# Optimization experiments

Hardware: AMD Instinct MI355X
Metric: run time of the kernel (lower is better)

The kernel has to match this reference:

```python
import jax, jax.numpy as jnp
import numpy as np

LOG2 = float(np.log(2.0))

def ssp(v):
    # shifted softplus: log(0.5*e^v + 0.5)
    return jax.nn.softplus(v) - jnp.asarray(LOG2, v.dtype)

def lora_dense(h, W, b, A, B):
    # base GEMM + per-sample (modulated) low-rank correction; scale = alpha/rank = 1
    base = jnp.einsum('b...i,io->b...o', h, W) + b
    lora = jnp.einsum('b...r,bro->b...o', jnp.einsum('b...i,bir->b...r', h, A), B)
    return ssp(base + lora)

def setup_inputs() -> dict:
    key = jax.random.key(0)
    ks = jax.random.split(key, 32)
    Bsz, Atoms, F, Rbf, R = 2, 512, 128, 64, 4
    d = {}
    d['x'] = jax.random.normal(ks[0], (Bsz, Atoms, F), jnp.float32)
    d['f_ij'] = jax.random.uniform(ks[1], (Bsz, Atoms, Atoms, Rbf), jnp.float32)
    d['c_ij'] = jax.random.uniform(ks[2], (Bsz, Atoms, Atoms), jnp.float32)
    d['mask'] = jax.random.randint(ks[3], (Bsz, Atoms, Atoms), 0, 2, jnp.int32)
    def mk(i, din, dout):
        return (jax.random.normal(ks[4+4*i], (din, dout), jnp.float32) * (1.0/np.sqrt(din)),
                jnp.zeros((dout,), jnp.float32),
                jax.random.normal(ks[5+4*i], (Bsz, din, R), jnp.float32) * 0.05,
                jax.random.normal(ks[6+4*i], (Bsz, R, dout), jnp.float32) * 0.05)
    d['W_bc'], d['b_bc'], d['A_bc'], d['B_bc'] = mk(0, F, F)      # atomwise_bc: F -> dim_filter(=F)
    d['W_f0'], d['b_f0'], d['A_f0'], d['B_f0'] = mk(1, Rbf, F)    # dis_filter layer0
    d['W_f1'], d['b_f1'], d['A_f1'], d['B_f1'] = mk(2, F, F)      # dis_filter layer1
    d['W_f2'], d['b_f2'], d['A_f2'], d['B_f2'] = mk(3, F, F)      # dis_filter layer2
    d['W_a0'], d['b_a0'], d['A_a0'], d['B_a0'] = mk(4, F, F)      # atomwise_ac layer0
    d['W_a1'], d['b_a1'], d['A_a1'], d['B_a1'] = mk(5, F, F)      # atomwise_ac layer1
    return d

def reference(x, f_ij, c_ij, mask,
              W_bc, b_bc, A_bc, B_bc,
              W_f0, b_f0, A_f0, B_f0,
              W_f1, b_f1, A_f1, B_f1,
              W_f2, b_f2, A_f2, B_f2,
              W_a0, b_a0, A_a0, B_a0,
              W_a1, b_a1, A_a1, B_a1):
    x_i = lora_dense(x, W_bc, b_bc, A_bc, B_bc)                 # (B, A, Fdim)
    h = lora_dense(f_ij, W_f0, b_f0, A_f0, B_f0)                # (B, A, A, Fdim)
    h = lora_dense(h, W_f1, b_f1, A_f1, B_f1)
    h = lora_dense(h, W_f2, b_f2, A_f2, B_f2)
    w_ij = h * c_ij[..., None]                                  # (B, A, A, Fdim)
    # x_ij = expand_dims(x_i, -3): neighbor-j features broadcast over receiver i
    y = x_i[:, None, :, :] * w_ij                               # (B, A, A, Fdim)
    y = y * mask[..., None].astype(y.dtype)
    y = jnp.sum(y, axis=-2)                                     # masked neighbor sum -> (B, A, Fdim)
    y = lora_dense(y, W_a0, b_a0, A_a0, B_a0)
    y = lora_dense(y, W_a1, b_a1, A_a1, B_a1)
    return x + y
```

## Files before the change

kernel.cpp:

```cpp
#include <hip/hip_runtime.h>
#include <hip/hip_bf16.h>


typedef float        f32x4  __attribute__((ext_vector_type(4)));
typedef unsigned int u32x4  __attribute__((ext_vector_type(4)));
typedef unsigned int u32x2  __attribute__((ext_vector_type(2)));
typedef __bf16       bf16x8 __attribute__((ext_vector_type(8)));

__device__ __forceinline__ float ssp_pre(float acc, float bpre) {
  float t = __builtin_amdgcn_exp2f(__builtin_fmaf(acc, 1.44269504089f, bpre));
  return 0.69314718056f * __builtin_amdgcn_logf(__builtin_fmaf(t, 0.5f, 0.5f));
}

__device__ __forceinline__ float ssp_f(float v) {
  float t = __builtin_amdgcn_exp2f(v * 1.44269504089f);
  return 0.69314718056f * __builtin_amdgcn_logf(__builtin_fmaf(t, 0.5f, 0.5f));
}

__device__ __forceinline__ unsigned short f2bfu(float f) {
  __hip_bfloat16 h = __float2bfloat16(f);
  return __builtin_bit_cast(unsigned short, h);
}

__device__ __forceinline__ u32x4 pack8(f32x4 a, f32x4 b) {
  u32x4 u;
  u.x = (unsigned)f2bfu(a.x) | ((unsigned)f2bfu(a.y) << 16);
  u.y = (unsigned)f2bfu(a.z) | ((unsigned)f2bfu(a.w) << 16);
  u.z = (unsigned)f2bfu(b.x) | ((unsigned)f2bfu(b.y) << 16);
  u.w = (unsigned)f2bfu(b.z) | ((unsigned)f2bfu(b.w) << 16);
  return u;
}

__device__ __forceinline__ f32x4 fzero4() { f32x4 z = {0.f, 0.f, 0.f, 0.f}; return z; }

#define SWZ(j) (((j) & 7) << 4)

__global__ void prep_weights(
    const float* __restrict__ W_bc, const float* __restrict__ A_bc, const float* __restrict__ B_bc,
    const float* __restrict__ W_f0, const float* __restrict__ A_f0, const float* __restrict__ B_f0,
    const float* __restrict__ W_f1, const float* __restrict__ A_f1, const float* __restrict__ B_f1,
    const float* __restrict__ W_f2, const float* __restrict__ A_f2, const float* __restrict__ B_f2,
    const float* __restrict__ W_a0, const float* __restrict__ A_a0, const float* __restrict__ B_a0,
    const float* __restrict__ W_a1, const float* __restrict__ A_a1, const float* __restrict__ B_a1,
    unsigned short* __restrict__ Wt0, unsigned short* __restrict__ Wt1, unsigned short* __restrict__ Wt2,
    float* __restrict__ Wbc, float* __restrict__ Wa0, float* __restrict__ Wa1)
{
  const int l = blockIdx.y, b = blockIdx.z;
  const int e = blockIdx.x * 256 + threadIdx.x;
  const float *W, *A, *Bm; int din;
  switch (l) {
    case 0:  W = W_bc; A = A_bc; Bm = B_bc; din = 128; break;
    case 1:  W = W_f0; A = A_f0; Bm = B_f0; din = 64;  break;
    case 2:  W = W_f1; A = A_f1; Bm = B_f1; din = 128; break;
    case 3:  W = W_f2; A = A_f2; Bm = B_f2; din = 128; break;
    case 4:  W = W_a0; A = A_a0; Bm = B_a0; din = 128; break;
    default: W = W_a1; A = A_a1; Bm = B_a1; din = 128; break;
  }
  if (e >= din * 128) return;
  const int k = e >> 7, n = e & 127;
  float wv = W[k * 128 + n];
  #pragma unroll
  for (int r = 0; r < 4; ++r)
    wv += A[(b * din + k) * 4 + r] * Bm[(b * 4 + r) * 128 + n];
  if (l == 1)      Wt0[(b * 128 + n) * 64  + k] = f2bfu(wv);
  else if (l == 2) Wt1[(b * 128 + n) * 128 + k] = f2bfu(wv);
  else if (l == 3) Wt2[(b * 128 + n) * 128 + k] = f2bfu(wv);
  else if (l == 0) Wbc[(b * 128 + k) * 128 + n] = wv;
  else if (l == 4) Wa0[(b * 128 + k) * 128 + n] = wv;
  else             Wa1[(b * 128 + k) * 128 + n] = wv;
}

__global__ __launch_bounds__(512) void dense_ssp(
    const float* __restrict__ in, const float* __restrict__ W,
    const float* __restrict__ bias, float* __restrict__ out)
{
  __shared__ float in_l[4][128];
  const int t = threadIdx.x;
  const int rg0 = blockIdx.x << 2;
  const int b = rg0 >> 9;
  in_l[t >> 7][t & 127] = in[rg0 * 128 + t];
  __syncthreads();
  const int j = t >> 7, n = t & 127;
  const float* wp = W + (b << 14) + n;
  const float* ip = in_l[j];
  float acc = 0.f;
  #pragma unroll 8
  for (int k = 0; k < 128; ++k) acc += ip[k] * wp[k << 7];
  out[(rg0 + j) * 128 + n] = ssp_f(acc + bias[n]);
}

__global__ __launch_bounds__(512) void dense2_ssp(
    const float* __restrict__ in, const float* __restrict__ in2,
    const float* __restrict__ W0, const float* __restrict__ b0,
    const float* __restrict__ W1, const float* __restrict__ b1,
    const float* __restrict__ resid, float* __restrict__ out)
{
  __shared__ float in_l[4][128];
  __shared__ float h_l[4][128];
  const int t = threadIdx.x;
  const int rg0 = blockIdx.x << 2;
  const int b = rg0 >> 9;
  in_l[t >> 7][t & 127] = in[rg0 * 128 + t] + in2[rg0 * 128 + t];
  __syncthreads();
  const int j = t >> 7, n = t & 127;
  {
    const float* wp = W0 + (b << 14) + n;
    const float* ip = in_l[j];
    float acc = 0.f;
    #pragma unroll 8
    for (int k = 0; k < 128; ++k) acc += ip[k] * wp[k << 7];
    h_l[j][n] = ssp_f(acc + b0[n]);
  }
  __syncthreads();
  {
    const float* wp = W1 + (b << 14) + n;
    const float* ip = h_l[j];
    float acc = 0.f;
    #pragma unroll 8
    for (int k = 0; k < 128; ++k) acc += ip[k] * wp[k << 7];
    const int oi = (rg0 + j) * 128 + n;
    out[oi] = ssp_f(acc + b1[n]) + resid[oi];
  }
}

__global__ __launch_bounds__(256, 4) void schnet_core(
    const float* __restrict__ f_ij, const float* __restrict__ c_ij,
    const int* __restrict__ mask,
    const unsigned short* __restrict__ Wt0, const unsigned short* __restrict__ Wt1,
    const unsigned short* __restrict__ Wt2,
    const float* __restrict__ bias0, const float* __restrict__ bias1,
    const float* __restrict__ bias2,
    const float* __restrict__ xi, float* __restrict__ ypart)
{
  __shared__ __align__(16) unsigned short fbuf[64 * 64];
  __shared__ __align__(16) unsigned short hbuf[64 * 128];
  __shared__ int   jlist[320];
  __shared__ float slist[320];
  __shared__ float bias_l[384];
  __shared__ int cnt_s[4], base_s[4], nact_s;

  const int tid  = threadIdx.x;
  const int lane = tid & 63;
  const int w    = tid >> 6;
  const int lrow = lane & 15;
  const int lgrp = lane >> 4;
  const int g    = blockIdx.x;
  const int bi   = g >> 1;
  const int h    = g & 1;
  const int b    = bi >> 9;

  for (int t = tid; t < 384; t += 256) {
    const float* bp = (t < 128) ? bias0 : (t < 256) ? bias1 : bias2;
    bias_l[t] = bp[t & 127] * 1.44269504089f;
  }

  const int mb = bi << 9;
  const int jg = (h << 8) + tid;
  const int   mA = mask[mb + jg];
  const float cA = c_ij[mb + jg];
  unsigned long long bal = __ballot(mA != 0);
  if (lane == 0) cnt_s[w] = __popcll(bal);
  __syncthreads();
  if (tid == 0) {
    int s = 0;
    for (int c = 0; c < 4; ++c) { base_s[c] = s; s += cnt_s[c]; }
    nact_s = s;
  }
  __syncthreads();
  const int na = nact_s;
  const unsigned long long lm = (1ull << lane) - 1ull;
  if (mA) { int p = base_s[w] + __popcll(bal & lm); jlist[p] = jg; slist[p] = cA; }
  if (tid < 64) { int idx = na + tid; if (idx < 320) { jlist[idx] = 0; slist[idx] = 0.f; } }
  __syncthreads();

  const int tiles = (na + 63) >> 6;

  const int mg = w;
  const float* fbase = f_ij + ((size_t)mb << 6);

  const int wbase0 = ((b << 7) + mg * 32 + lrow) * 64  + (lgrp << 3);
  const int wbase1 = ((b << 7) + mg * 32 + lrow) * 128 + (lgrp << 3);

  float accy[2][4] = {{0.f,0.f,0.f,0.f},{0.f,0.f,0.f,0.f}};

  bf16x8 wfA[2][2];
  {
    const unsigned short* wp = Wt0 + wbase0;
    #pragma unroll
    for (int nt = 0; nt < 2; ++nt)
      #pragma unroll
      for (int ks = 0; ks < 2; ++ks)
        wfA[nt][ks] = *(const bf16x8*)(wp + nt * (16 * 64) + ks * 32);
  }

  const int r    = tid >> 2;
  const int part = tid & 3;
  f32x4 pre0, pre1, pre2, pre3;
  {
    const int ja = jlist[r];
    const f32x4* src = (const f32x4*)(fbase + ja * 64 + part * 16);
    pre0 = src[0]; pre1 = src[1]; pre2 = src[2]; pre3 = src[3];
  }

  for (int tt = 0; tt < tiles; ++tt) {
    const int jt0 = tt << 6;
    {
      char* dst = (char*)fbuf + r * 128;
      const int o0 = (part * 32) ^ SWZ(r);
      *(u32x4*)(dst + o0)        = pack8(pre0, pre1);
      *(u32x4*)(dst + (o0 ^ 16)) = pack8(pre2, pre3);
    }
    __syncthreads();

    if (tt + 1 < tiles) {
      const int ja = jlist[((tt + 1) << 6) + r];
      const f32x4* src = (const f32x4*)(fbase + ja * 64 + part * 16);
      pre0 = src[0]; pre1 = src[1]; pre2 = src[2]; pre3 = src[3];
    }

    f32x4 acc[2][4];

    #pragma unroll
    for (int nt = 0; nt < 2; ++nt)
      #pragma unroll
      for (int jt = 0; jt < 4; ++jt) acc[nt][jt] = fzero4();
    #pragma unroll
    for (int jt = 0; jt < 4; ++jt) {
      const int j = jt * 16 + lrow;
      const char* rb = (const char*)fbuf + j * 128;
      const int sw = SWZ(j);
      #pragma unroll
      for (int ks = 0; ks < 2; ++ks) {
        bf16x8 bf = *(const bf16x8*)(rb + ((lgrp * 16 + ks * 64) ^ sw));
        acc[0][jt] = __builtin_amdgcn_mfma_f32_16x16x32_bf16(wfA[0][ks], bf, acc[0][jt], 0, 0, 0);
        acc[1][jt] = __builtin_amdgcn_mfma_f32_16x16x32_bf16(wfA[1][ks], bf, acc[1][jt], 0, 0, 0);
      }
    }

    bf16x8 wfB[2][4];
    {
      const unsigned short* wp = Wt1 + wbase1;
      asm volatile("" : "+v"(wp));
      #pragma unroll
      for (int nt = 0; nt < 2; ++nt)
        #pragma unroll
        for (int ks = 0; ks < 4; ++ks)
          wfB[nt][ks] = *(const bf16x8*)(wp + nt * (16 * 128) + ks * 32);
    }

    {
      f32x4 bp0 = *(const f32x4*)(bias_l + mg * 32 + 0  + lgrp * 4);
      f32x4 bp1 = *(const f32x4*)(bias_l + mg * 32 + 16 + lgrp * 4);
      #pragma unroll
      for (int jt = 0; jt < 4; ++jt) {
        const int j = jt * 16 + lrow;
        char* rb = (char*)hbuf + j * 256;
        const int sw = SWZ(j);
        #pragma unroll
        for (int nt = 0; nt < 2; ++nt) {
          const int n0 = mg * 32 + nt * 16 + lgrp * 4;
          const f32x4 bp = nt ? bp1 : bp0;
          float e0 = ssp_pre(acc[nt][jt].x, bp.x);
          float e1 = ssp_pre(acc[nt][jt].y, bp.y);
          float e2 = ssp_pre(acc[nt][jt].z, bp.z);
          float e3 = ssp_pre(acc[nt][jt].w, bp.w);
          u32x2 pk;
          pk.x = (unsigned)f2bfu(e0) | ((unsigned)f2bfu(e1) << 16);
          pk.y = (unsigned)f2bfu(e2) | ((unsigned)f2bfu(e3) << 16);
          *(u32x2*)(rb + ((n0 * 2) ^ sw)) = pk;
        }
      }
    }
    __syncthreads();

    #pragma unroll
    for (int nt = 0; nt < 2; ++nt)
      #pragma unroll
      for (int jt = 0; jt < 4; ++jt) acc[nt][jt] = fzero4();
    #pragma unroll
    for (int jt = 0; jt < 4; ++jt) {
      const int j = jt * 16 + lrow;
      const char* rb = (const char*)hbuf + j * 256;
      const int sw = SWZ(j);
      #pragma unroll
      for (int ks = 0; ks < 4; ++ks) {
        bf16x8 bf = *(const bf16x8*)(rb + ((lgrp * 16 + ks * 64) ^ sw));
        acc[0][jt] = __builtin_amdgcn_mfma_f32_16x16x32_bf16(wfB[0][ks], bf, acc[0][jt], 0, 0, 0);
        acc[1][jt] = __builtin_amdgcn_mfma_f32_16x16x32_bf16(wfB[1][ks], bf, acc[1][jt], 0, 0, 0);
      }
    }
    __syncthreads();

    bf16x8 wfC[2][4];
    {
      const unsigned short* wp = Wt2 + wbase1;
      asm volatile("" : "+v"(wp));
      #pragma unroll
      for (int nt = 0; nt < 2; ++nt)
        #pragma unroll
        for (int ks = 0; ks < 4; ++ks)
          wfC[nt][ks] = *(const bf16x8*)(wp + nt * (16 * 128) + ks * 32);
    }

    {
      f32x4 bp0 = *(const f32x4*)(bias_l + 128 + mg * 32 + 0  + lgrp * 4);
      f32x4 bp1 = *(const f32x4*)(bias_l + 128 + mg * 32 + 16 + lgrp * 4);
      #pragma unroll
      for (int jt = 0; jt < 4; ++jt) {
        const int j = jt * 16 + lrow;
        char* rb = (char*)hbuf + j * 256;
        const int sw = SWZ(j);
        #pragma unroll
        for (int nt = 0; nt < 2; ++nt) {
          const int n0 = mg * 32 + nt * 16 + lgrp * 4;
          const f32x4 bp = nt ? bp1 : bp0;
          float e0 = ssp_pre(acc[nt][jt].x, bp.x);
          float e1 = ssp_pre(acc[nt][jt].y, bp.y);
          float e2 = ssp_pre(acc[nt][jt].z, bp.z);
          float e3 = ssp_pre(acc[nt][jt].w, bp.w);
          u32x2 pk;
          pk.x = (unsigned)f2bfu(e0) | ((unsigned)f2bfu(e1) << 16);
          pk.y = (unsigned)f2bfu(e2) | ((unsigned)f2bfu(e3) << 16);
          *(u32x2*)(rb + ((n0 * 2) ^ sw)) = pk;
        }
      }
    }
    __syncthreads();

    #pragma unroll
    for (int nt = 0; nt < 2; ++nt)
      #pragma unroll
      for (int jt = 0; jt < 4; ++jt) acc[nt][jt] = fzero4();
    #pragma unroll
    for (int jt = 0; jt < 4; ++jt) {
      const int j = jt * 16 + lrow;
      const char* rb = (const char*)hbuf + j * 256;
      const int sw = SWZ(j);
      #pragma unroll
      for (int ks = 0; ks < 4; ++ks) {
        bf16x8 bf = *(const bf16x8*)(rb + ((lgrp * 16 + ks * 64) ^ sw));
        acc[0][jt] = __builtin_amdgcn_mfma_f32_16x16x32_bf16(wfC[0][ks], bf, acc[0][jt], 0, 0, 0);
        acc[1][jt] = __builtin_amdgcn_mfma_f32_16x16x32_bf16(wfC[1][ks], bf, acc[1][jt], 0, 0, 0);
      }
    }

    {
      const unsigned short* wp = Wt0 + wbase0;
      asm volatile("" : "+v"(wp));
      #pragma unroll
      for (int nt = 0; nt < 2; ++nt)
        #pragma unroll
        for (int ks = 0; ks < 2; ++ks)
          wfA[nt][ks] = *(const bf16x8*)(wp + nt * (16 * 64) + ks * 32);
    }

    {
      f32x4 bp0 = *(const f32x4*)(bias_l + 256 + mg * 32 + 0  + lgrp * 4);
      f32x4 bp1 = *(const f32x4*)(bias_l + 256 + mg * 32 + 16 + lgrp * 4);
      #pragma unroll
      for (int jt = 0; jt < 4; ++jt) {
        const int jj = jt * 16 + lrow;
        const float s  = slist[jt0 + jj];
        const int   ja = jlist[jt0 + jj];
        const float* xr = xi + (((b << 9) + ja) << 7);
        #pragma unroll
        for (int nt = 0; nt < 2; ++nt) {
          const int n0 = mg * 32 + nt * 16 + lgrp * 4;
          const f32x4 bp = nt ? bp1 : bp0;
          f32x4 xv = *(const f32x4*)(xr + n0);
          float h0 = ssp_pre(acc[nt][jt].x, bp.x);
          float h1 = ssp_pre(acc[nt][jt].y, bp.y);
          float h2 = ssp_pre(acc[nt][jt].z, bp.z);
          float h3 = ssp_pre(acc[nt][jt].w, bp.w);
          accy[nt][0] += s * xv.x * h0;
          accy[nt][1] += s * xv.y * h1;
          accy[nt][2] += s * xv.z * h2;
          accy[nt][3] += s * xv.w * h3;
        }
      }
    }
  }

  #pragma unroll
  for (int d = 1; d < 16; d <<= 1)
    #pragma unroll
    for (int nt = 0; nt < 2; ++nt)
      #pragma unroll
      for (int rr = 0; rr < 4; ++rr)
        accy[nt][rr] += __shfl_xor(accy[nt][rr], d, 64);
  if (lrow == 0) {
    float* yo = ypart + ((size_t)h << 17) + ((size_t)bi << 7);
    #pragma unroll
    for (int nt = 0; nt < 2; ++nt) {
      const int n0 = mg * 32 + nt * 16 + lgrp * 4;
      f32x4 v = {accy[nt][0], accy[nt][1], accy[nt][2], accy[nt][3]};
      *(f32x4*)(yo + n0) = v;
    }
  }
}

extern "C" void kernel_launch(void* const* d_in, const int* in_sizes, int n_in,
                              void* d_out, int out_size, void* d_ws, size_t ws_size,
                              hipStream_t stream)
{
  const float* x    = (const float*)d_in[0];
  const float* f_ij = (const float*)d_in[1];
  const float* c_ij = (const float*)d_in[2];
  const int*   mask = (const int*)d_in[3];
  const float* W_bc = (const float*)d_in[4];
  const float* b_bc = (const float*)d_in[5];
  const float* A_bc = (const float*)d_in[6];
  const float* B_bc = (const float*)d_in[7];
  const float* W_f0 = (const float*)d_in[8];
  const float* b_f0 = (const float*)d_in[9];
  const float* A_f0 = (const float*)d_in[10];
  const float* B_f0 = (const float*)d_in[11];
  const float* W_f1 = (const float*)d_in[12];
  const float* b_f1 = (const float*)d_in[13];
  const float* A_f1 = (const float*)d_in[14];
  const float* B_f1 = (const float*)d_in[15];
  const float* W_f2 = (const float*)d_in[16];
  const float* b_f2 = (const float*)d_in[17];
  const float* A_f2 = (const float*)d_in[18];
  const float* B_f2 = (const float*)d_in[19];
  const float* W_a0 = (const float*)d_in[20];
  const float* b_a0 = (const float*)d_in[21];
  const float* A_a0 = (const float*)d_in[22];
  const float* B_a0 = (const float*)d_in[23];
  const float* W_a1 = (const float*)d_in[24];
  const float* b_a1 = (const float*)d_in[25];
  const float* A_a1 = (const float*)d_in[26];
  const float* B_a1 = (const float*)d_in[27];
  float* out = (float*)d_out;

  char* ws = (char*)d_ws;
  unsigned short* Wt0 = (unsigned short*)(ws);
  unsigned short* Wt1 = (unsigned short*)(ws + 32768);
  unsigned short* Wt2 = (unsigned short*)(ws + 98304);
  float* Wbc = (float*)(ws + 163840);
  float* Wa0 = (float*)(ws + 294912);
  float* Wa1 = (float*)(ws + 425984);
  float* xi  = (float*)(ws + 557056);
  float* yp  = (float*)(ws + 1081344);

  prep_weights<<<dim3(64, 6, 2), 256, 0, stream>>>(
      W_bc, A_bc, B_bc, W_f0, A_f0, B_f0, W_f1, A_f1, B_f1,
      W_f2, A_f2, B_f2, W_a0, A_a0, B_a0, W_a1, A_a1, B_a1,
      Wt0, Wt1, Wt2, Wbc, Wa0, Wa1);

  dense_ssp<<<256, 512, 0, stream>>>(x, Wbc, b_bc, xi);

  schnet_core<<<2048, 256, 0, stream>>>(f_ij, c_ij, mask, Wt0, Wt1, Wt2,
                                        b_f0, b_f1, b_f2, xi, yp);

  dense2_ssp<<<256, 512, 0, stream>>>(yp, yp + (1 << 17), Wa0, b_a0,
                                      Wa1, b_a1, x, out);
}
```

Baseline: 112.9 us.

## Merge neighbor halves per block, fold ssp constants into weights, skip empty subtiles

Each block now handles all 512 neighbors of one receiver atom instead of splitting them across two blocks. This removes the partial-sum buffer and the extra add in the final dense stage. The shifted-softplus is simplified algebraically: the ln2 and 0.5 factors are folded into the layer-1/2 weights, the biases and the c_ij scale, leaving exp2 plus log2 per element. 16-row subtiles past the active-neighbor count are skipped, and the hbuf swizzle is widened to 16 rows to cut LDS bank conflicts. Trade-off: fewer blocks (1024) means less parallelism, and a single block per atom runs longer.

```diff
diff --git a/kernel.cpp b/kernel.cpp
--- a/kernel.cpp
+++ b/kernel.cpp
@@ -7,14 +7,17 @@
 typedef unsigned int u32x2  __attribute__((ext_vector_type(2)));
 typedef __bf16       bf16x8 __attribute__((ext_vector_type(8)));
 
+#define LOG2E 1.44269504089f
+#define LN2   0.69314718056f
+
 __device__ __forceinline__ float ssp_pre(float acc, float bpre) {
-  float t = __builtin_amdgcn_exp2f(__builtin_fmaf(acc, 1.44269504089f, bpre));
-  return 0.69314718056f * __builtin_amdgcn_logf(__builtin_fmaf(t, 0.5f, 0.5f));
+  float t = __builtin_amdgcn_exp2f(__builtin_fmaf(acc, LOG2E, bpre));
+  return __builtin_amdgcn_logf(t + 0.5f);
 }
 
 __device__ __forceinline__ float ssp_f(float v) {
-  float t = __builtin_amdgcn_exp2f(v * 1.44269504089f);
-  return 0.69314718056f * __builtin_amdgcn_logf(__builtin_fmaf(t, 0.5f, 0.5f));
+  float t = __builtin_amdgcn_exp2f(v * LOG2E);
+  return LN2 * __builtin_amdgcn_logf(__builtin_fmaf(t, 0.5f, 0.5f));
 }
 
 __device__ __forceinline__ unsigned short f2bfu(float f) {
@@ -33,7 +36,8 @@
 
 __device__ __forceinline__ f32x4 fzero4() { f32x4 z = {0.f, 0.f, 0.f, 0.f}; return z; }
 
-#define SWZ(j) (((j) & 7) << 4)
+#define SWZF(j) (((j) & 7) << 4)
+#define SWZH(j) (((j) & 15) << 4)
 
 __global__ void prep_weights(
     const float* __restrict__ W_bc, const float* __restrict__ A_bc, const float* __restrict__ B_bc,
@@ -63,8 +67,8 @@
   for (int r = 0; r < 4; ++r)
     wv += A[(b * din + k) * 4 + r] * Bm[(b * 4 + r) * 128 + n];
   if (l == 1)      Wt0[(b * 128 + n) * 64  + k] = f2bfu(wv);
-  else if (l == 2) Wt1[(b * 128 + n) * 128 + k] = f2bfu(wv);
-  else if (l == 3) Wt2[(b * 128 + n) * 128 + k] = f2bfu(wv);
+  else if (l == 2) Wt1[(b * 128 + n) * 128 + k] = f2bfu(wv * LN2);
+  else if (l == 3) Wt2[(b * 128 + n) * 128 + k] = f2bfu(wv * LN2);
   else if (l == 0) Wbc[(b * 128 + k) * 128 + n] = wv;
   else if (l == 4) Wa0[(b * 128 + k) * 128 + n] = wv;
   else             Wa1[(b * 128 + k) * 128 + n] = wv;
@@ -90,7 +94,7 @@
 }
 
 __global__ __launch_bounds__(512) void dense2_ssp(
-    const float* __restrict__ in, const float* __restrict__ in2,
+    const float* __restrict__ in,
     const float* __restrict__ W0, const float* __restrict__ b0,
     const float* __restrict__ W1, const float* __restrict__ b1,
     const float* __restrict__ resid, float* __restrict__ out)
@@ -100,7 +104,7 @@
   const int t = threadIdx.x;
   const int rg0 = blockIdx.x << 2;
   const int b = rg0 >> 9;
-  in_l[t >> 7][t & 127] = in[rg0 * 128 + t] + in2[rg0 * 128 + t];
+  in_l[t >> 7][t & 127] = in[rg0 * 128 + t];
   __syncthreads();
   const int j = t >> 7, n = t & 127;
   {
@@ -130,47 +134,47 @@
     const unsigned short* __restrict__ Wt2,
     const float* __restrict__ bias0, const float* __restrict__ bias1,
     const float* __restrict__ bias2,
-    const float* __restrict__ xi, float* __restrict__ ypart)
+    const float* __restrict__ xi, float* __restrict__ y)
 {
   __shared__ __align__(16) unsigned short fbuf[64 * 64];
   __shared__ __align__(16) unsigned short hbuf[64 * 128];
-  __shared__ int   jlist[320];
-  __shared__ float slist[320];
+  __shared__ int   jlist[576];
+  __shared__ float slist[576];
   __shared__ float bias_l[384];
-  __shared__ int cnt_s[4], base_s[4], nact_s;
+  __shared__ int cnt_s[8], base_s[8], nact_s;
 
   const int tid  = threadIdx.x;
   const int lane = tid & 63;
   const int w    = tid >> 6;
   const int lrow = lane & 15;
   const int lgrp = lane >> 4;
-  const int g    = blockIdx.x;
-  const int bi   = g >> 1;
-  const int h    = g & 1;
+  const int bi   = blockIdx.x;
   const int b    = bi >> 9;
 
   for (int t = tid; t < 384; t += 256) {
     const float* bp = (t < 128) ? bias0 : (t < 256) ? bias1 : bias2;
-    bias_l[t] = bp[t & 127] * 1.44269504089f;
+    bias_l[t] = __builtin_fmaf(bp[t & 127], LOG2E, -1.0f);
   }
 
   const int mb = bi << 9;
-  const int jg = (h << 8) + tid;
-  const int   mA = mask[mb + jg];
-  const float cA = c_ij[mb + jg];
-  unsigned long long bal = __ballot(mA != 0);
-  if (lane == 0) cnt_s[w] = __popcll(bal);
+  const int jA = tid, jB = tid + 256;
+  const int   mA = mask[mb + jA]; const float cA = c_ij[mb + jA];
+  const int   mB = mask[mb + jB]; const float cB = c_ij[mb + jB];
+  unsigned long long balA = __ballot(mA != 0);
+  unsigned long long balB = __ballot(mB != 0);
+  if (lane == 0) { cnt_s[w] = __popcll(balA); cnt_s[4 + w] = __popcll(balB); }
   __syncthreads();
   if (tid == 0) {
     int s = 0;
-    for (int c = 0; c < 4; ++c) { base_s[c] = s; s += cnt_s[c]; }
+    for (int c = 0; c < 8; ++c) { base_s[c] = s; s += cnt_s[c]; }
     nact_s = s;
   }
   __syncthreads();
   const int na = nact_s;
   const unsigned long long lm = (1ull << lane) - 1ull;
-  if (mA) { int p = base_s[w] + __popcll(bal & lm); jlist[p] = jg; slist[p] = cA; }
-  if (tid < 64) { int idx = na + tid; if (idx < 320) { jlist[idx] = 0; slist[idx] = 0.f; } }
+  if (mA) { int p = base_s[w]     + __popcll(balA & lm); jlist[p] = jA; slist[p] = cA * LN2; }
+  if (mB) { int p = base_s[4 + w] + __popcll(balB & lm); jlist[p] = jB; slist[p] = cB * LN2; }
+  if (tid < 64) { int idx = na + tid; if (idx < 576) { jlist[idx] = 0; slist[idx] = 0.f; } }
   __syncthreads();
 
   const int tiles = (na + 63) >> 6;
@@ -204,9 +208,11 @@
 
   for (int tt = 0; tt < tiles; ++tt) {
     const int jt0 = tt << 6;
+    const int jcnt = na - jt0;
+
     {
       char* dst = (char*)fbuf + r * 128;
-      const int o0 = (part * 32) ^ SWZ(r);
+      const int o0 = (part * 32) ^ SWZF(r);
       *(u32x4*)(dst + o0)        = pack8(pre0, pre1);
       *(u32x4*)(dst + (o0 ^ 16)) = pack8(pre2, pre3);
     }
@@ -226,14 +232,16 @@
       for (int jt = 0; jt < 4; ++jt) acc[nt][jt] = fzero4();
     #pragma unroll
     for (int jt = 0; jt < 4; ++jt) {
-      const int j = jt * 16 + lrow;
-      const char* rb = (const char*)fbuf + j * 128;
-      const int sw = SWZ(j);
-      #pragma unroll
-      for (int ks = 0; ks < 2; ++ks) {
-        bf16x8 bf = *(const bf16x8*)(rb + ((lgrp * 16 + ks * 64) ^ sw));
-        acc[0][jt] = __builtin_amdgcn_mfma_f32_16x16x32_bf16(wfA[0][ks], bf, acc[0][jt], 0, 0, 0);
-        acc[1][jt] = __builtin_amdgcn_mfma_f32_16x16x32_bf16(wfA[1][ks], bf, acc[1][jt], 0, 0, 0);
+      if (jt * 16 < jcnt) {
+        const int j = jt * 16 + lrow;
+        const char* rb = (const char*)fbuf + j * 128;
+        const int sw = SWZF(j);
+        #pragma unroll
+        for (int ks = 0; ks < 2; ++ks) {
+          bf16x8 bf = *(const bf16x8*)(rb + ((lgrp * 16 + ks * 64) ^ sw));
+          acc[0][jt] = __builtin_amdgcn_mfma_f32_16x16x32_bf16(wfA[0][ks], bf, acc[0][jt], 0, 0, 0);
+          acc[1][jt] = __builtin_amdgcn_mfma_f32_16x16x32_bf16(wfA[1][ks], bf, acc[1][jt], 0, 0, 0);
+        }
       }
     }
 
@@ -253,40 +261,44 @@
       f32x4 bp1 = *(const f32x4*)(bias_l + mg * 32 + 16 + lgrp * 4);
       #pragma unroll
       for (int jt = 0; jt < 4; ++jt) {
+        if (jt * 16 < jcnt) {
+          const int j = jt * 16 + lrow;
+          char* rb = (char*)hbuf + j * 256;
+          const int sw = SWZH(j);
+          #pragma unroll
+          for (int nt = 0; nt < 2; ++nt) {
+            const int n0 = mg * 32 + nt * 16 + lgrp * 4;
+            const f32x4 bp = nt ? bp1 : bp0;
+            float e0 = ssp_pre(acc[nt][jt].x, bp.x);
+            float e1 = ssp_pre(acc[nt][jt].y, bp.y);
+            float e2 = ssp_pre(acc[nt][jt].z, bp.z);
+            float e3 = ssp_pre(acc[nt][jt].w, bp.w);
+            u32x2 pk;
+            pk.x = (unsigned)f2bfu(e0) | ((unsigned)f2bfu(e1) << 16);
+            pk.y = (unsigned)f2bfu(e2) | ((unsigned)f2bfu(e3) << 16);
+            *(u32x2*)(rb + ((n0 * 2) ^ sw)) = pk;
+          }
+        }
+      }
+    }
+    __syncthreads();
+
+    #pragma unroll
+    for (int nt = 0; nt < 2; ++nt)
+      #pragma unroll
+      for (int jt = 0; jt < 4; ++jt) acc[nt][jt] = fzero4();
+    #pragma unroll
+    for (int jt = 0; jt < 4; ++jt) {
+      if (jt * 16 < jcnt) {
         const int j = jt * 16 + lrow;
-        char* rb = (char*)hbuf + j * 256;
-        const int sw = SWZ(j);
-        #pragma unroll
-        for (int nt = 0; nt < 2; ++nt) {
-          const int n0 = mg * 32 + nt * 16 + lgrp * 4;
-          const f32x4 bp = nt ? bp1 : bp0;
-          float e0 = ssp_pre(acc[nt][jt].x, bp.x);
-          float e1 = ssp_pre(acc[nt][jt].y, bp.y);
-          float e2 = ssp_pre(acc[nt][jt].z, bp.z);
-          float e3 = ssp_pre(acc[nt][jt].w, bp.w);
-          u32x2 pk;
-          pk.x = (unsigned)f2bfu(e0) | ((unsigned)f2bfu(e1) << 16);
-          pk.y = (unsigned)f2bfu(e2) | ((unsigned)f2bfu(e3) << 16);
-          *(u32x2*)(rb + ((n0 * 2) ^ sw)) = pk;
-        }
-      }
-    }
-    __syncthreads();
-
-    #pragma unroll
-    for (int nt = 0; nt < 2; ++nt)
-      #pragma unroll
-      for (int jt = 0; jt < 4; ++jt) acc[nt][jt] = fzero4();
-    #pragma unroll
-    for (int jt = 0; jt < 4; ++jt) {
-      const int j = jt * 16 + lrow;
-      const char* rb = (const char*)hbuf + j * 256;
-      const int sw = SWZ(j);
-      #pragma unroll
-      for (int ks = 0; ks < 4; ++ks) {
-        bf16x8 bf = *(const bf16x8*)(rb + ((lgrp * 16 + ks * 64) ^ sw));
-        acc[0][jt] = __builtin_amdgcn_mfma_f32_16x16x32_bf16(wfB[0][ks], bf, acc[0][jt], 0, 0, 0);
-        acc[1][jt] = __builtin_amdgcn_mfma_f32_16x16x32_bf16(wfB[1][ks], bf, acc[1][jt], 0, 0, 0);
+        const char* rb = (const char*)hbuf + j * 256;
+        const int sw = SWZH(j);
+        #pragma unroll
+        for (int ks = 0; ks < 4; ++ks) {
+          bf16x8 bf = *(const bf16x8*)(rb + ((lgrp * 16 + ks * 64) ^ sw));
+          acc[0][jt] = __builtin_amdgcn_mfma_f32_16x16x32_bf16(wfB[0][ks], bf, acc[0][jt], 0, 0, 0);
+          acc[1][jt] = __builtin_amdgcn_mfma_f32_16x16x32_bf16(wfB[1][ks], bf, acc[1][jt], 0, 0, 0);
+        }
       }
     }
     __syncthreads();
@@ -307,40 +319,44 @@
       f32x4 bp1 = *(const f32x4*)(bias_l + 128 + mg * 32 + 16 + lgrp * 4);
       #pragma unroll
       for (int jt = 0; jt < 4; ++jt) {
+        if (jt * 16 < jcnt) {
+          const int j = jt * 16 + lrow;
+          char* rb = (char*)hbuf + j * 256;
+          const int sw = SWZH(j);
+          #pragma unroll
+          for (int nt = 0; nt < 2; ++nt) {
+            const int n0 = mg * 32 + nt * 16 + lgrp * 4;
+            const f32x4 bp = nt ? bp1 : bp0;
+            float e0 = ssp_pre(acc[nt][jt].x, bp.x);
+            float e1 = ssp_pre(acc[nt][jt].y, bp.y);
+            float e2 = ssp_pre(acc[nt][jt].z, bp.z);
+            float e3 = ssp_pre(acc[nt][jt].w, bp.w);
+            u32x2 pk;
+            pk.x = (unsigned)f2bfu(e0) | ((unsigned)f2bfu(e1) << 16);
+            pk.y = (unsigned)f2bfu(e2) | ((unsigned)f2bfu(e3) << 16);
+            *(u32x2*)(rb + ((n0 * 2) ^ sw)) = pk;
+          }
+        }
+      }
+    }
+    __syncthreads();
+
+    #pragma unroll
+    for (int nt = 0; nt < 2; ++nt)
+      #pragma unroll
+      for (int jt = 0; jt < 4; ++jt) acc[nt][jt] = fzero4();
+    #pragma unroll
+    for (int jt = 0; jt < 4; ++jt) {
+      if (jt * 16 < jcnt) {
         const int j = jt * 16 + lrow;
-        char* rb = (char*)hbuf + j * 256;
-        const int sw = SWZ(j);
-        #pragma unroll
-        for (int nt = 0; nt < 2; ++nt) {
-          const int n0 = mg * 32 + nt * 16 + lgrp * 4;
-          const f32x4 bp = nt ? bp1 : bp0;
-          float e0 = ssp_pre(acc[nt][jt].x, bp.x);
-          float e1 = ssp_pre(acc[nt][jt].y, bp.y);
-          float e2 = ssp_pre(acc[nt][jt].z, bp.z);
-          float e3 = ssp_pre(acc[nt][jt].w, bp.w);
-          u32x2 pk;
-          pk.x = (unsigned)f2bfu(e0) | ((unsigned)f2bfu(e1) << 16);
-          pk.y = (unsigned)f2bfu(e2) | ((unsigned)f2bfu(e3) << 16);
-          *(u32x2*)(rb + ((n0 * 2) ^ sw)) = pk;
-        }
-      }
-    }
-    __syncthreads();
-
-    #pragma unroll
-    for (int nt = 0; nt < 2; ++nt)
-      #pragma unroll
-      for (int jt = 0; jt < 4; ++jt) acc[nt][jt] = fzero4();
-    #pragma unroll
-    for (int jt = 0; jt < 4; ++jt) {
-      const int j = jt * 16 + lrow;
-      const char* rb = (const char*)hbuf + j * 256;
-      const int sw = SWZ(j);
-      #pragma unroll
-      for (int ks = 0; ks < 4; ++ks) {
-        bf16x8 bf = *(const bf16x8*)(rb + ((lgrp * 16 + ks * 64) ^ sw));
-        acc[0][jt] = __builtin_amdgcn_mfma_f32_16x16x32_bf16(wfC[0][ks], bf, acc[0][jt], 0, 0, 0);
-        acc[1][jt] = __builtin_amdgcn_mfma_f32_16x16x32_bf16(wfC[1][ks], bf, acc[1][jt], 0, 0, 0);
+        const char* rb = (const char*)hbuf + j * 256;
+        const int sw = SWZH(j);
+        #pragma unroll
+        for (int ks = 0; ks < 4; ++ks) {
+          bf16x8 bf = *(const bf16x8*)(rb + ((lgrp * 16 + ks * 64) ^ sw));
+          acc[0][jt] = __builtin_amdgcn_mfma_f32_16x16x32_bf16(wfC[0][ks], bf, acc[0][jt], 0, 0, 0);
+          acc[1][jt] = __builtin_amdgcn_mfma_f32_16x16x32_bf16(wfC[1][ks], bf, acc[1][jt], 0, 0, 0);
+        }
       }
     }
 
@@ -359,23 +375,25 @@
       f32x4 bp1 = *(const f32x4*)(bias_l + 256 + mg * 32 + 16 + lgrp * 4);
       #pragma unroll
       for (int jt = 0; jt < 4; ++jt) {
-        const int jj = jt * 16 + lrow;
-        const float s  = slist[jt0 + jj];
-        const int   ja = jlist[jt0 + jj];
-        const float* xr = xi + (((b << 9) + ja) << 7);
-        #pragma unroll
-        for (int nt = 0; nt < 2; ++nt) {
-          const int n0 = mg * 32 + nt * 16 + lgrp * 4;
-          const f32x4 bp = nt ? bp1 : bp0;
-          f32x4 xv = *(const f32x4*)(xr + n0);
-          float h0 = ssp_pre(acc[nt][jt].x, bp.x);
-          float h1 = ssp_pre(acc[nt][jt].y, bp.y);
-          float h2 = ssp_pre(acc[nt][jt].z, bp.z);
-          float h3 = ssp_pre(acc[nt][jt].w, bp.w);
-          accy[nt][0] += s * xv.x * h0;
-          accy[nt][1] += s * xv.y * h1;
-          accy[nt][2] += s * xv.z * h2;
-          accy[nt][3] += s * xv.w * h3;
+        if (jt * 16 < jcnt) {
+          const int jj = jt * 16 + lrow;
+          const float s  = slist[jt0 + jj];
+          const int   ja = jlist[jt0 + jj];
+          const float* xr = xi + (((b << 9) + ja) << 7);
+          #pragma unroll
+          for (int nt = 0; nt < 2; ++nt) {
+            const int n0 = mg * 32 + nt * 16 + lgrp * 4;
+            const f32x4 bp = nt ? bp1 : bp0;
+            f32x4 xv = *(const f32x4*)(xr + n0);
+            float h0 = ssp_pre(acc[nt][jt].x, bp.x);
+            float h1 = ssp_pre(acc[nt][jt].y, bp.y);
+            float h2 = ssp_pre(acc[nt][jt].z, bp.z);
+            float h3 = ssp_pre(acc[nt][jt].w, bp.w);
+            accy[nt][0] += s * xv.x * h0;
+            accy[nt][1] += s * xv.y * h1;
+            accy[nt][2] += s * xv.z * h2;
+            accy[nt][3] += s * xv.w * h3;
+          }
         }
       }
     }
@@ -389,7 +407,7 @@
       for (int rr = 0; rr < 4; ++rr)
         accy[nt][rr] += __shfl_xor(accy[nt][rr], d, 64);
   if (lrow == 0) {
-    float* yo = ypart + ((size_t)h << 17) + ((size_t)bi << 7);
+    float* yo = y + ((size_t)bi << 7);
     #pragma unroll
     for (int nt = 0; nt < 2; ++nt) {
       const int n0 = mg * 32 + nt * 16 + lgrp * 4;
@@ -450,9 +468,8 @@
 
   dense_ssp<<<256, 512, 0, stream>>>(x, Wbc, b_bc, xi);
 
-  schnet_core<<<2048, 256, 0, stream>>>(f_ij, c_ij, mask, Wt0, Wt1, Wt2,
+  schnet_core<<<1024, 256, 0, stream>>>(f_ij, c_ij, mask, Wt0, Wt1, Wt2,
                                         b_f0, b_f1, b_f2, xi, yp);
 
-  dense2_ssp<<<256, 512, 0, stream>>>(yp, yp + (1 << 17), Wa0, b_a0,
-                                      Wa1, b_a1, x, out);
-}
+  dense2_ssp<<<256, 512, 0, stream>>>(yp, Wa0, b_a0, Wa1, b_a1, x, out);
+}
```

After: 97.31 us (median of 2 runs). 13.8% less time.
